# Optimization experiments

Measured on AMD Instinct MI355X. Metric: run time of the kernel, lower is better.

Reference implementation:

```python
import jax, jax.numpy as jnp
import numpy as np

T, B, E, H, V = 50, 64, 1024, 1024, 32000
NL = 2


def setup_inputs() -> dict:
    key = jax.random.key(0)
    ks = jax.random.split(key, 16)
    def rn(k, shape, fan_in):
        return jax.random.normal(k, shape, jnp.float32) * (1.0 / np.sqrt(fan_in))
    return {
        "word": jax.random.randint(ks[0], (B,), 0, V),
        "seq": jax.random.randint(ks[1], (T, B), 0, V),
        "emb": jax.random.normal(ks[2], (V, E), jnp.float32) * 0.05,
        "w2h_W": rn(ks[3], (H, E), E),
        "w2h_b": jnp.zeros((H,), jnp.float32),
        "W_ih0": rn(ks[4], (4 * H, 2 * E), 2 * E),
        "W_hh0": rn(ks[5], (4 * H, H), H),
        "b_ih0": jnp.zeros((4 * H,), jnp.float32),
        "b_hh0": jnp.zeros((4 * H,), jnp.float32),
        "W_ih1": rn(ks[6], (4 * H, H), H),
        "W_hh1": rn(ks[7], (4 * H, H), H),
        "b_ih1": jnp.zeros((4 * H,), jnp.float32),
        "b_hh1": jnp.zeros((4 * H,), jnp.float32),
        "dec_W": rn(ks[8], (V, H), H),
        "dec_b": jnp.zeros((V,), jnp.float32),
    }


def _lstm_layer(x, Wih, Whh, bih, bhh, h0, c0):
    """x: [T,B,D] -> hs: [T,B,H]. PyTorch gate order: i,f,g,o."""
    b = bih + bhh
    # precompute input contribution for all timesteps (one big GEMM)
    xg = jnp.einsum('tbd,gd->tbg', x, Wih) + b  # [T,B,4H]

    def step(carry, xt):
        h, c = carry
        gates = xt + h @ Whh.T
        i, f, g, o = jnp.split(gates, 4, axis=-1)
        c = jax.nn.sigmoid(f) * c + jax.nn.sigmoid(i) * jnp.tanh(g)
        h = jax.nn.sigmoid(o) * jnp.tanh(c)
        return (h, c), h

    (hT, cT), hs = jax.lax.scan(step, (h0, c0), xg)
    return hs, hT, cT


def reference(word, seq, emb, w2h_W, w2h_b, W_ih0, W_hh0, b_ih0, b_hh0,
              W_ih1, W_hh1, b_ih1, b_hh1, dec_W, dec_b):
    word_emb = emb[word]            # [B,E]
    seq_emb = emb[seq]              # [T,B,E]
    # init_hidden: c = word2hidden(word_emb) expanded over layers, h = zeros
    c0 = word_emb @ w2h_W.T + w2h_b          # [B,H]
    h0 = jnp.zeros_like(c0)
    # use_input: concat word_emb to every timestep input
    x0 = jnp.concatenate(
        [jnp.broadcast_to(word_emb[None], (T, B, E)), seq_emb], axis=-1)  # [T,B,2E]
    hs0, h0T, c0T = _lstm_layer(x0, W_ih0, W_hh0, b_ih0, b_hh0, h0, c0)
    hs1, h1T, c1T = _lstm_layer(hs0, W_ih1, W_hh1, b_ih1, b_hh1, h0, c0)
    outputs = hs1.reshape(T * B, H)
    decoded = outputs @ dec_W.T + dec_b      # [T*B, V]
    h_final = jnp.stack([h0T, h1T], 0)       # [NL,B,H]
    c_final = jnp.stack([c0T, c1T], 0)
    return decoded, h_final, c_final
```

## Files before the change

### kernel.cpp

```cpp
#include <hip/hip_runtime.h>
#include <cstddef>


static constexpr int T_ = 50, B_ = 64, E_ = 1024, H_ = 1024, V_ = 32000;
static constexpr int G_ = 4096;

typedef unsigned short u16;
typedef unsigned int u32;
typedef unsigned long long u64;
typedef __attribute__((ext_vector_type(8))) short bf16x8;
typedef __attribute__((ext_vector_type(8))) unsigned short u16x8;
typedef __attribute__((ext_vector_type(4))) float f32x4;

__device__ __forceinline__ int perm_g(int n) {
  return ((n >> 4) & 3) * H_ + (n >> 6) * 16 + (n & 15);
}
__device__ __forceinline__ u16 bf16_rn(float x) {
  union { float f; unsigned u; } a; a.f = x;
  unsigned r = a.u + 0x7fffu + ((a.u >> 16) & 1u);
  return (u16)(r >> 16);
}
__device__ __forceinline__ float bf16_f(u16 h) {
  union { float f; unsigned u; } a; a.u = ((unsigned)h) << 16;
  return a.f;
}
__device__ __forceinline__ float sigm(float x) { return 1.f / (1.f + __expf(-x)); }

__global__ void fill_zero(float* p, int n) {
  int i = blockIdx.x * blockDim.x + threadIdx.x;
  if (i < n) p[i] = 0.f;
}
__global__ void bias_perm(const float* a, const float* b, float* dst) {
  int n = blockIdx.x * 256 + threadIdx.x;
  int s = perm_g(n);
  dst[n] = a[s] + b[s];
}

__global__ void conv_w(const float* __restrict__ src, int srcld, int coloff,
                       const int* __restrict__ gidx, int PERM, int rows,
                       u16* __restrict__ dst) {
  int idx = blockIdx.x * 256 + threadIdx.x;
  int r = idx >> 7, kc = (idx & 127) << 3;
  if (r >= rows) return;
  int s = gidx ? gidx[r] : (PERM ? perm_g(r) : r);
  const float* p = src + (size_t)s * srcld + coloff + kc;
  float4 v0 = *(const float4*)p, v1 = *(const float4*)(p + 4);
  float vv[8] = {v0.x, v0.y, v0.z, v0.w, v1.x, v1.y, v1.z, v1.w};
  u16 hi[8], lo[8];
#pragma unroll
  for (int i = 0; i < 8; ++i) {
    hi[i] = bf16_rn(vv[i]);
    lo[i] = bf16_rn(vv[i] - bf16_f(hi[i]));
  }
  u16x8 c0, c1;
#pragma unroll
  for (int i = 0; i < 4; ++i) {
    c0[2 * i] = hi[i];     c0[2 * i + 1] = lo[i];
    c1[2 * i] = hi[4 + i]; c1[2 * i + 1] = lo[4 + i];
  }
  int seg = kc >> 5;
  int ch0 = (kc >> 2) & 7;
  size_t base = (size_t)r * 2048 + seg * 64;
  *(u16x8*)&dst[base + (size_t)((ch0 ^ (r & 7)) << 3)] = c0;
  *(u16x8*)&dst[base + (size_t)(((ch0 | 1) ^ (r & 7)) << 3)] = c1;
}

template<int BM, int BN, int BK, int TM, int TN>
__launch_bounds__(256)
__global__ void gemm_nt(
    const float* __restrict__ A, const int* __restrict__ Aidx, int lda,
    const float* __restrict__ W, int ldw, int koff,
    const float* __restrict__ bias, float* __restrict__ C, int ldc,
    int M, int N, int K) {
  constexpr int TX = BN / TN;
  constexpr int TY = BM / TM;
  static_assert(TX * TY == 256, "thread geometry");
  __shared__ float As[BK][BM + 4];
  __shared__ float Ws[BK][BN + 4];
  const int tid = threadIdx.x;
  const int tx = tid % TX, ty = tid / TX;
  const int m0 = blockIdx.y * BM, n0 = blockIdx.x * BN;
  float acc[TM][TN];
#pragma unroll
  for (int i = 0; i < TM; ++i)
#pragma unroll
    for (int j = 0; j < TN; ++j) acc[i][j] = 0.f;
  constexpr int AV = (BM * BK) / 4;
  constexpr int WV = (BN * BK) / 4;
  constexpr int KV = BK / 4;
  for (int k0 = 0; k0 < K; k0 += BK) {
#pragma unroll
    for (int lp = 0; lp < (AV + 255) / 256; ++lp) {
      int e = tid + lp * 256;
      if (e < AV) {
        int r = e / KV, kq = e % KV;
        int m = m0 + r;
        float4 v = make_float4(0.f, 0.f, 0.f, 0.f);
        if (m < M) {
          int row = Aidx ? Aidx[m] : m;
          v = *(const float4*)&A[(size_t)row * lda + k0 + kq * 4];
        }
        As[kq * 4 + 0][r] = v.x; As[kq * 4 + 1][r] = v.y;
        As[kq * 4 + 2][r] = v.z; As[kq * 4 + 3][r] = v.w;
      }
    }
#pragma unroll
    for (int lp = 0; lp < (WV + 255) / 256; ++lp) {
      int e = tid + lp * 256;
      if (e < WV) {
        int cc = e / KV, kq = e % KV;
        int n = n0 + cc;
        float4 v = make_float4(0.f, 0.f, 0.f, 0.f);
        if (n < N)
          v = *(const float4*)&W[(size_t)n * ldw + koff + k0 + kq * 4];
        Ws[kq * 4 + 0][cc] = v.x; Ws[kq * 4 + 1][cc] = v.y;
        Ws[kq * 4 + 2][cc] = v.z; Ws[kq * 4 + 3][cc] = v.w;
      }
    }
    __syncthreads();
#pragma unroll
    for (int kk = 0; kk < BK; ++kk) {
      float a[TM], b[TN];
#pragma unroll
      for (int i = 0; i < TM; ++i) a[i] = As[kk][ty * TM + i];
#pragma unroll
      for (int j = 0; j < TN; ++j) b[j] = Ws[kk][tx * TN + j];
#pragma unroll
      for (int i = 0; i < TM; ++i)
#pragma unroll
        for (int j = 0; j < TN; ++j)
          acc[i][j] += a[i] * b[j];
    }
    __syncthreads();
  }
#pragma unroll
  for (int i = 0; i < TM; ++i) {
    int m = m0 + ty * TM + i;
    if (m >= M) continue;
#pragma unroll
    for (int j = 0; j < TN; ++j) {
      int n = n0 + tx * TN + j;
      if (n >= N) continue;
      float v = acc[i][j];
      if (bias) v += bias[n];
      C[(size_t)m * ldc + n] = v;
    }
  }
}

__launch_bounds__(256)
__global__ void gemm_bt(const u16* __restrict__ A, int Mrows,
                        const u16* __restrict__ Wb,
                        const float* __restrict__ bias,
                        const float* __restrict__ Dadd, int ldd, int dmask,
                        float* __restrict__ C, int ldc, int N, int nbx,
                        int mt, int ord) {
  __shared__ u16 lsA[128 * 64];
  __shared__ u16 lsB[128 * 64];

  int nwg = gridDim.x, bid = blockIdx.x;
  int q = nwg >> 3, r = nwg & 7;
  int xcd = bid & 7, base = bid >> 3;
  int wg = (xcd < r ? xcd * (q + 1) : r * (q + 1) + (xcd - r) * q) + base;
  int bx, by;
  if (ord) { by = wg % mt; bx = wg / mt; } else { bx = wg % nbx; by = wg / nbx; }
  const int m0 = by * 128, n0 = bx * 128;

  const int tid = threadIdx.x, w = tid >> 6, l = tid & 63;
  const int lr = l & 15, lq = l >> 4;
  const int wm = (w >> 1) * 64, wn = (w & 1) * 64;

  f32x4 acc[4][4] = {};

  for (int kt = 0; kt < 32; ++kt) {
#pragma unroll
    for (int i = 0; i < 4; ++i) {
      int rb = w * 32 + i * 8;
      int gm = m0 + rb + (l >> 3);
      if (gm > Mrows - 1) gm = Mrows - 1;
      const u16* ga = A + (size_t)gm * 2048 + kt * 64 + (l & 7) * 8;
      __builtin_amdgcn_global_load_lds(
          (const __attribute__((address_space(1))) void*)ga,
          (__attribute__((address_space(3))) void*)(lsA + rb * 64), 16, 0, 0);
      const u16* gb = Wb + (size_t)(n0 + rb + (l >> 3)) * 2048 + kt * 64 + (l & 7) * 8;
      __builtin_amdgcn_global_load_lds(
          (const __attribute__((address_space(1))) void*)gb,
          (__attribute__((address_space(3))) void*)(lsB + rb * 64), 16, 0, 0);
    }
    asm volatile("s_waitcnt vmcnt(0)" ::: "memory");
    __syncthreads();

    bf16x8 af[4][2], bfr[4][2];
#pragma unroll
    for (int i = 0; i < 4; ++i) {
      int ar = wm + i * 16 + lr;
#pragma unroll
      for (int s = 0; s < 2; ++s)
        af[i][s] = *(const bf16x8*)&lsA[ar * 64 + (((s << 2) + lq) ^ (ar & 7)) * 8];
    }
#pragma unroll
    for (int j = 0; j < 4; ++j) {
      int br = wn + j * 16 + lr;
#pragma unroll
      for (int s = 0; s < 2; ++s)
        bfr[j][s] = *(const bf16x8*)&lsB[br * 64 + (((s << 2) + lq) ^ (br & 7)) * 8];
    }
#pragma unroll
    for (int i = 0; i < 4; ++i)
#pragma unroll
      for (int j = 0; j < 4; ++j) {
        acc[i][j] = __builtin_amdgcn_mfma_f32_16x16x32_bf16(af[i][0], bfr[j][0], acc[i][j], 0, 0, 0);
        acc[i][j] = __builtin_amdgcn_mfma_f32_16x16x32_bf16(af[i][1], bfr[j][1], acc[i][j], 0, 0, 0);
      }
    __syncthreads();
  }

#pragma unroll
  for (int i = 0; i < 4; ++i) {
    int mbase = m0 + wm + i * 16 + lq * 4;
#pragma unroll
    for (int j = 0; j < 4; ++j) {
      int n = n0 + wn + j * 16 + lr;
      float badd = bias ? bias[n] : 0.f;
#pragma unroll
      for (int rr = 0; rr < 4; ++rr) {
        int m = mbase + rr;
        if (m >= Mrows) continue;
        float v = acc[i][j][rr] + badd;
        if (Dadd) {
          int dr = (dmask < 0) ? m : (m & dmask);
          v += Dadd[(size_t)dr * ldd + n];
        }
        C[(size_t)m * ldc + n] = v;
      }
    }
  }
}

__launch_bounds__(256)
__global__ void gemm_sp(
    const float* __restrict__ A, int lda,
    const float* __restrict__ W, int ldw,
    const float* __restrict__ bias,
    float* __restrict__ C, int ldc, int M, int N, int K, int nbx) {
  __shared__ u16 As_h[128][40], As_l[128][40];
  __shared__ u16 Ws_h[128][40], Ws_l[128][40];
  int nwg = gridDim.x, bid = blockIdx.x;
  int q = nwg >> 3, r = nwg & 7;
  int xcd = bid & 7, base = bid >> 3;
  int wg = (xcd < r ? xcd * (q + 1) : r * (q + 1) + (xcd - r) * q) + base;
  int bx = wg % nbx, by = wg / nbx;
  const int m0 = by * 128, n0 = bx * 128;
  const int tid = threadIdx.x;
  const int wave = tid >> 6, lane = tid & 63;
  const int lr = lane & 15, lq = lane >> 4;
  const int wm = (wave >> 1) * 64, wn = (wave & 1) * 64;
  f32x4 acc[4][4] = {};
  for (int k0 = 0; k0 < K; k0 += 32) {
#pragma unroll
    for (int lp = 0; lp < 4; ++lp) {
      int s = tid + lp * 256;
      int row = s >> 3, kq = s & 7;
      float4 v = make_float4(0.f, 0.f, 0.f, 0.f);
      int gm = m0 + row;
      if (gm < M)
        v = *(const float4*)&A[(size_t)gm * lda + k0 + kq * 4];
      u16 h0 = bf16_rn(v.x), h1 = bf16_rn(v.y), h2 = bf16_rn(v.z), h3 = bf16_rn(v.w);
      u16 l0 = bf16_rn(v.x - bf16_f(h0)), l1 = bf16_rn(v.y - bf16_f(h1));
      u16 l2 = bf16_rn(v.z - bf16_f(h2)), l3 = bf16_rn(v.w - bf16_f(h3));
      *(uint2*)&As_h[row][kq * 4] =
          make_uint2((u32)h0 | ((u32)h1 << 16), (u32)h2 | ((u32)h3 << 16));
      *(uint2*)&As_l[row][kq * 4] =
          make_uint2((u32)l0 | ((u32)l1 << 16), (u32)l2 | ((u32)l3 << 16));
    }
#pragma unroll
    for (int lp = 0; lp < 4; ++lp) {
      int s = tid + lp * 256;
      int col = s >> 3, kq = s & 7;
      int n = n0 + col;
      float4 v = make_float4(0.f, 0.f, 0.f, 0.f);
      if (n < N)
        v = *(const float4*)&W[(size_t)n * ldw + k0 + kq * 4];
      u16 h0 = bf16_rn(v.x), h1 = bf16_rn(v.y), h2 = bf16_rn(v.z), h3 = bf16_rn(v.w);
      u16 l0 = bf16_rn(v.x - bf16_f(h0)), l1 = bf16_rn(v.y - bf16_f(h1));
      u16 l2 = bf16_rn(v.z - bf16_f(h2)), l3 = bf16_rn(v.w - bf16_f(h3));
      *(uint2*)&Ws_h[col][kq * 4] =
          make_uint2((u32)h0 | ((u32)h1 << 16), (u32)h2 | ((u32)h3 << 16));
      *(uint2*)&Ws_l[col][kq * 4] =
          make_uint2((u32)l0 | ((u32)l1 << 16), (u32)l2 | ((u32)l3 << 16));
    }
    __syncthreads();
    bf16x8 ah[4], al[4], bh[4], bl[4];
#pragma unroll
    for (int i = 0; i < 4; ++i) {
      ah[i] = *(const bf16x8*)&As_h[wm + i * 16 + lr][lq * 8];
      al[i] = *(const bf16x8*)&As_l[wm + i * 16 + lr][lq * 8];
    }
#pragma unroll
    for (int j = 0; j < 4; ++j) {
      bh[j] = *(const bf16x8*)&Ws_h[wn + j * 16 + lr][lq * 8];
      bl[j] = *(const bf16x8*)&Ws_l[wn + j * 16 + lr][lq * 8];
    }
#pragma unroll
    for (int i = 0; i < 4; ++i)
#pragma unroll
      for (int j = 0; j < 4; ++j) {
        acc[i][j] = __builtin_amdgcn_mfma_f32_16x16x32_bf16(ah[i], bh[j], acc[i][j], 0, 0, 0);
        acc[i][j] = __builtin_amdgcn_mfma_f32_16x16x32_bf16(ah[i], bl[j], acc[i][j], 0, 0, 0);
        acc[i][j] = __builtin_amdgcn_mfma_f32_16x16x32_bf16(al[i], bh[j], acc[i][j], 0, 0, 0);
      }
    __syncthreads();
  }
#pragma unroll
  for (int i = 0; i < 4; ++i) {
    int mbase = m0 + wm + i * 16 + lq * 4;
#pragma unroll
    for (int j = 0; j < 4; ++j) {
      int n = n0 + wn + j * 16 + lr;
      if (n >= N) continue;
      float badd = bias ? bias[n] : 0.f;
#pragma unroll
      for (int rr = 0; rr < 4; ++rr) {
        int m = mbase + rr;
        if (m >= M) continue;
        C[(size_t)m * ldc + n] = acc[i][j][rr] + badd;
      }
    }
  }
}

__device__ __forceinline__ void gemm_half(
    const u32* __restrict__ hp, int rg, int w, int lr, int lq,
    const bf16x8 (&bfr)[8][4], f32x4 (&acc)[2][4]) {
  bf16x8 af[8][2];
#pragma unroll
  for (int s = 0; s < 8; ++s)
#pragma unroll
    for (int mt = 0; mt < 2; ++mt) {
      int m = rg * 32 + mt * 16 + lr;
      int seg = w * 4 + (s >> 1);
      int cis = ((((s & 1) << 2) + lq) ^ (lr & 7));
      const u32* p = hp + (size_t)m * 1024 + seg * 32 + cis * 4;
      asm volatile("global_load_dwordx4 %0, %1, off sc0 sc1"
                   : "=v"(af[s][mt]) : "v"(p) : "memory");
    }
  asm volatile("s_waitcnt vmcnt(0)" ::: "memory");
  __builtin_amdgcn_sched_barrier(0);
#pragma unroll
  for (int s = 0; s < 8; ++s)
#pragma unroll
    for (int mt = 0; mt < 2; ++mt)
#pragma unroll
      for (int nt = 0; nt < 4; ++nt)
        acc[mt][nt] = __builtin_amdgcn_mfma_f32_16x16x32_bf16(
            af[s][mt], bfr[s][nt], acc[mt][nt], 0, 0, 0);
}

__device__ __forceinline__ void poll_flags(const u32* flags, int rg, int l, u32 tgt) {
  int guard = 0;
  for (;;) {
    u32 v = __hip_atomic_load(flags + (size_t)((rg << 6) + l) * 4,
                              __ATOMIC_RELAXED, __HIP_MEMORY_SCOPE_AGENT);
    if (__all(v >= tgt)) break;
    if (++guard > (1 << 23)) break;
    __builtin_amdgcn_s_sleep(1);
  }
}

__device__ void decoder_block(char* smem, int dblk,
                              const u32* __restrict__ h1s,
                              const float* __restrict__ decW,
                              const float* __restrict__ dec_b,
                              const u32* __restrict__ flg1,
                              float* __restrict__ outC, int tid) {
  u16* As = (u16*)smem;
  u16* Bs = (u16*)(smem + 32768);
  const int w = tid >> 6, l = tid & 63;
  const int lr = l & 15, lq = l >> 4;
  const int n0 = dblk * 128;
  const u16* h1u = (const u16*)h1s;
  const int wmL = (w >> 1) * 64, wnL = (w & 1) * 64;

  for (int ch = 0; ch < 13; ++ch) {
    const int nSl = (ch < 12) ? 4 : 2;
    const int nrows = nSl * 64;
    const u32 tgt = (u32)(4 * ch + nSl);
    if (w == 0) { poll_flags(flg1, 0, l, tgt); poll_flags(flg1, 1, l, tgt); }
    __syncthreads();

    f32x4 acc[4][4] = {};
    for (int kt = 0; kt < 32; ++kt) {
#pragma unroll
      for (int i = 0; i < 4; ++i) {
        int rb = w * 32 + i * 8;
        int rl = rb + (l >> 3);
        int gm = rl < nrows ? rl : nrows - 1;
        int slot = 4 * ch + 1 + (gm >> 6);
        const u16* ga = h1u + (size_t)slot * (64 * 2048) +
                        (size_t)(gm & 63) * 2048 + kt * 64 + (l & 7) * 8;
        __builtin_amdgcn_global_load_lds(
            (const __attribute__((address_space(1))) void*)ga,
            (__attribute__((address_space(3))) void*)(As + rb * 64), 16, 0, 0);
      }
      {
        int row = tid >> 2, kq8 = (tid & 3) * 8;
        const float* p = decW + (size_t)(n0 + row) * 1024 + kt * 32 + kq8;
        float4 v0 = *(const float4*)p, v1 = *(const float4*)(p + 4);
        float vv[8] = {v0.x, v0.y, v0.z, v0.w, v1.x, v1.y, v1.z, v1.w};
        u16 hi[8], lo[8];
#pragma unroll
        for (int q2 = 0; q2 < 8; ++q2) {
          hi[q2] = bf16_rn(vv[q2]);
          lo[q2] = bf16_rn(vv[q2] - bf16_f(hi[q2]));
        }
        u16x8 c0, c1;
#pragma unroll
        for (int q2 = 0; q2 < 4; ++q2) {
          c0[2 * q2] = hi[q2];     c0[2 * q2 + 1] = lo[q2];
          c1[2 * q2] = hi[4 + q2]; c1[2 * q2 + 1] = lo[4 + q2];
        }
        int c0i = kq8 >> 2;
        u16* dst = Bs + row * 64;
        *(u16x8*)&dst[(c0i ^ (row & 7)) << 3] = c0;
        *(u16x8*)&dst[((c0i | 1) ^ (row & 7)) << 3] = c1;
      }
      asm volatile("s_waitcnt vmcnt(0)" ::: "memory");
      __syncthreads();

      bf16x8 af[4][2], bfr[4][2];
#pragma unroll
      for (int i = 0; i < 4; ++i) {
        int ar = wmL + i * 16 + lr;
#pragma unroll
        for (int s = 0; s < 2; ++s)
          af[i][s] = *(const bf16x8*)&As[ar * 64 + (((s << 2) + lq) ^ (ar & 7)) * 8];
      }
#pragma unroll
      for (int j = 0; j < 4; ++j) {
        int br = wnL + j * 16 + lr;
#pragma unroll
        for (int s = 0; s < 2; ++s)
          bfr[j][s] = *(const bf16x8*)&Bs[br * 64 + (((s << 2) + lq) ^ (br & 7)) * 8];
      }
#pragma unroll
      for (int i = 0; i < 4; ++i)
#pragma unroll
        for (int j = 0; j < 4; ++j) {
          acc[i][j] = __builtin_amdgcn_mfma_f32_16x16x32_bf16(af[i][0], bfr[j][0], acc[i][j], 0, 0, 0);
          acc[i][j] = __builtin_amdgcn_mfma_f32_16x16x32_bf16(af[i][1], bfr[j][1], acc[i][j], 0, 0, 0);
        }
      __syncthreads();
    }
#pragma unroll
    for (int i = 0; i < 4; ++i) {
      int mrow = wmL + i * 16 + lq * 4;
      if (mrow >= nrows) continue;
#pragma unroll
      for (int j = 0; j < 4; ++j) {
        int col = n0 + wnL + j * 16 + lr;
        float badd = dec_b[col];
#pragma unroll
        for (int rr = 0; rr < 4; ++rr)
          outC[(size_t)(ch * 256 + mrow + rr) * V_ + col] = acc[i][j][rr] + badd;
      }
    }
  }
}

template<bool DUAL, bool EMIT, bool DEC>
__launch_bounds__(512, 4)
__global__ void rnn_dual(const u16* __restrict__ Whh0b, const u16* __restrict__ Whh1b,
                         const u16* __restrict__ Wih1b,
                         const float* __restrict__ xg0all, const float* __restrict__ bias1p,
                         float* __restrict__ cL0, float* __restrict__ hL0,
                         float* __restrict__ cL1, float* __restrict__ hL1,
                         u32* __restrict__ h0s, u32* __restrict__ h1s,
                         float* __restrict__ hsf,
                         u32* __restrict__ flg0, u32* __restrict__ flg1,
                         const float* __restrict__ decW, const float* __restrict__ dec_b,
                         float* __restrict__ outC, int T) {
  __shared__ char smem[69632];
  float* partial = (float*)smem;

  const int bid = blockIdx.x;
  const int tid = threadIdx.x, w = tid >> 6, l = tid & 63;
  const int lr = l & 15, lq = l >> 4;

  if (DEC && bid >= 256) {
    decoder_block(smem, bid - 256, h1s, decW, dec_b, flg1, outC, tid);
    return;
  }

  const int x = bid & 7, j = bid >> 3;
  const int layer = DUAL ? (j & 1) : 0;
  const int idx = DUAL ? (j >> 1) : j;
  const int ct = x * 8 + (idx & 7);
  const int rg = idx >> 3;

  const u16* WbA = (layer ? Whh1b : Whh0b) + (size_t)(ct * 64) * 2048;
  bf16x8 bfragA[8][4];
#pragma unroll
  for (int s = 0; s < 8; ++s)
#pragma unroll
    for (int nt = 0; nt < 4; ++nt) {
      int row = nt * 16 + lr;
      int seg = w * 4 + (s >> 1);
      int cis = ((((s & 1) << 2) + lq) ^ (lr & 7));
      bfragA[s][nt] = *(const bf16x8*)&WbA[(size_t)row * 2048 + seg * 64 + cis * 8];
    }
  bf16x8 bfragX[8][4];
  if (DUAL && layer) {
    const u16* WbX = Wih1b + (size_t)(ct * 64) * 2048;
#pragma unroll
    for (int s = 0; s < 8; ++s)
#pragma unroll
      for (int nt = 0; nt < 4; ++nt) {
        int row = nt * 16 + lr;
        int seg = w * 4 + (s >> 1);
        int cis = ((((s & 1) << 2) + lq) ^ (lr & 7));
        bfragX[s][nt] = *(const bf16x8*)&WbX[(size_t)row * 2048 + seg * 64 + cis * 8];
      }
  }

  const int cm = tid >> 4, cu = tid & 15;
  const int m_c = rg * 32 + cm;
  const int unit = ct * 16 + cu;
  float* cL = layer ? cL1 : cL0;
  float* hL = layer ? hL1 : hL0;
  u32* hsl = layer ? h1s : h0s;
  u32* flgS = layer ? flg1 : flg0;
  float creg = cL[m_c * H_ + unit];
  float bset[4];
  if (layer) {
#pragma unroll
    for (int g = 0; g < 4; ++g)
      bset[g] = bias1p[ct * 64 + g * 16 + cu];
  }

  for (int t = 0; t < T; ++t) {
    float xgv[4];
    if (!layer) {
      const float* xg = xg0all + (size_t)t * ((size_t)B_ * G_);
#pragma unroll
      for (int g = 0; g < 4; ++g)
        xgv[g] = xg[(size_t)m_c * G_ + ct * 64 + g * 16 + cu];
    } else {
#pragma unroll
      for (int g = 0; g < 4; ++g) xgv[g] = bset[g];
    }

    f32x4 acc[2][4] = {};

    if (layer) {
      if (t && w == 0) poll_flags(flg1, rg, l, (u32)t);
      __syncthreads();
      gemm_half(h1s + (size_t)t * (B_ * 1024), rg, w, lr, lq, bfragA, acc);
      if (w == 0) poll_flags(flg0, rg, l, (u32)(t + 1));
      __syncthreads();
      gemm_half(h0s + (size_t)(t + 1) * (B_ * 1024), rg, w, lr, lq, bfragX, acc);
    } else {
      if (t && w == 0) poll_flags(flg0, rg, l, (u32)t);
      __syncthreads();
      gemm_half(h0s + (size_t)t * (B_ * 1024), rg, w, lr, lq, bfragA, acc);
    }

#pragma unroll
    for (int mt = 0; mt < 2; ++mt)
#pragma unroll
      for (int nt = 0; nt < 4; ++nt)
#pragma unroll
        for (int rr = 0; rr < 4; ++rr)
          partial[(w * 32 + mt * 16 + lq * 4 + rr) * 68 + nt * 16 + lr] = acc[mt][nt][rr];
    __syncthreads();

    float g4[4];
#pragma unroll
    for (int g = 0; g < 4; ++g) {
      float ssum = xgv[g];
#pragma unroll
      for (int p = 0; p < 8; ++p) ssum += partial[(p * 32 + cm) * 68 + g * 16 + cu];
      g4[g] = ssum;
    }
    float cn = sigm(g4[1]) * creg + sigm(g4[0]) * tanhf(g4[2]);
    float hn = sigm(g4[3]) * tanhf(cn);
    creg = cn;
    if (EMIT && layer) hsf[(size_t)t * (B_ * H_) + m_c * H_ + unit] = hn;
    if (t == T - 1) { cL[m_c * H_ + unit] = cn; hL[m_c * H_ + unit] = hn; }
    u16 hh = bf16_rn(hn);
    u16 hl2 = bf16_rn(hn - bf16_f(hh));
    u32 packed = (u32)hh | ((u32)hl2 << 16);
    u32* hnext = hsl + (size_t)(t + 1) * (B_ * 1024);
    u32 hidx = m_c * 1024 + ((unit >> 5) << 5) +
               ((((unit >> 2) & 7) ^ (m_c & 7)) << 2) + (unit & 3);
    {
      u32* sp = hnext + hidx;
      asm volatile("global_store_dword %0, %1, off sc0 sc1"
                   :: "v"(sp), "v"(packed) : "memory");
    }

    asm volatile("s_waitcnt vmcnt(0)" ::: "memory");
    __syncthreads();
    if (tid == 0)
      __hip_atomic_store(flgS + (size_t)((rg << 6) + ct) * 4, (u32)(t + 1),
                         __ATOMIC_RELAXED, __HIP_MEMORY_SCOPE_AGENT);
  }
}

__launch_bounds__(256)
__global__ void rnn_step(const u16* __restrict__ hprev, const u16* __restrict__ Wb,
                         const float* __restrict__ xg,
                         float* __restrict__ c, float* __restrict__ hf,
                         u32* __restrict__ hout) {
  __shared__ char smem[32768];
  u16* lsA = (u16*)smem;
  u16* lsB = (u16*)(smem + 16384);
  const int nt = blockIdx.x, n0 = nt * 64;
  const int tid = threadIdx.x, w = tid >> 6, l = tid & 63;
  const int lr = l & 15, lq = l >> 4;
  f32x4 acc[4] = {};
  for (int kt = 0; kt < 16; ++kt) {
#pragma unroll
    for (int i = 0; i < 4; ++i) {
      int rb = w * 16 + i * 4;
      const u16* ga = hprev + (size_t)(rb + (l >> 4)) * 2048 + kt * 128 + (l & 15) * 8;
      __builtin_amdgcn_global_load_lds(
          (const __attribute__((address_space(1))) void*)ga,
          (__attribute__((address_space(3))) void*)(lsA + rb * 128), 16, 0, 0);
      const u16* gb = Wb + (size_t)(n0 + rb + (l >> 4)) * 2048 + kt * 128 + (l & 15) * 8;
      __builtin_amdgcn_global_load_lds(
          (const __attribute__((address_space(1))) void*)gb,
          (__attribute__((address_space(3))) void*)(lsB + rb * 128), 16, 0, 0);
    }
    asm volatile("s_waitcnt vmcnt(0)" ::: "memory");
    __syncthreads();
    bf16x8 af[4];
    int ar = w * 16 + lr;
#pragma unroll
    for (int s = 0; s < 4; ++s)
      af[s] = *(const bf16x8*)&lsA[ar * 128 + (s >> 1) * 64 + ((((s & 1) << 2) + lq) ^ (ar & 7)) * 8];
#pragma unroll
    for (int jj = 0; jj < 4; ++jj) {
      int br = jj * 16 + lr;
#pragma unroll
      for (int s = 0; s < 4; ++s) {
        bf16x8 bv = *(const bf16x8*)&lsB[br * 128 + (s >> 1) * 64 + ((((s & 1) << 2) + lq) ^ (br & 7)) * 8];
        acc[jj] = __builtin_amdgcn_mfma_f32_16x16x32_bf16(af[s], bv, acc[jj], 0, 0, 0);
      }
    }
    __syncthreads();
  }
  float* gsh = (float*)smem;
#pragma unroll
  for (int jj = 0; jj < 4; ++jj)
#pragma unroll
    for (int rr = 0; rr < 4; ++rr)
      gsh[(w * 16 + lq * 4 + rr) * 68 + jj * 16 + lr] = acc[jj][rr];
  __syncthreads();
  const int ui = tid & 15, mq = tid >> 4;
#pragma unroll
  for (int mr = 0; mr < 4; ++mr) {
    int m = mr * 16 + mq;
    float gi = gsh[m * 68 + 0 + ui]  + xg[(size_t)m * G_ + n0 + 0 + ui];
    float gf = gsh[m * 68 + 16 + ui] + xg[(size_t)m * G_ + n0 + 16 + ui];
    float gg = gsh[m * 68 + 32 + ui] + xg[(size_t)m * G_ + n0 + 32 + ui];
    float go = gsh[m * 68 + 48 + ui] + xg[(size_t)m * G_ + n0 + 48 + ui];
    int unit = nt * 16 + ui;
    int ci = m * H_ + unit;
    float cn = sigm(gf) * c[ci] + sigm(gi) * tanhf(gg);
    float hn = sigm(go) * tanhf(cn);
    c[ci] = cn;
    hf[ci] = hn;
    u16 hh = bf16_rn(hn);
    u16 hl = bf16_rn(hn - bf16_f(hh));
    u32 hidx = m * 1024 + ((unit >> 5) << 5) +
               ((((unit >> 2) & 7) ^ (m & 7)) << 2) + (unit & 3);
    hout[hidx] = (u32)hh | ((u32)hl << 16);
  }
}

extern "C" void kernel_launch(void* const* d_in, const int* in_sizes, int n_in,
                              void* d_out, int out_size, void* d_ws, size_t ws_size,
                              hipStream_t stream) {
  const int*   word  = (const int*)  d_in[0];
  const int*   seq   = (const int*)  d_in[1];
  const float* emb   = (const float*)d_in[2];
  const float* w2h_W = (const float*)d_in[3];
  const float* w2h_b = (const float*)d_in[4];
  const float* W_ih0 = (const float*)d_in[5];
  const float* W_hh0 = (const float*)d_in[6];
  const float* b_ih0 = (const float*)d_in[7];
  const float* b_hh0 = (const float*)d_in[8];
  const float* W_ih1 = (const float*)d_in[9];
  const float* W_hh1 = (const float*)d_in[10];
  const float* b_ih1 = (const float*)d_in[11];
  const float* b_hh1 = (const float*)d_in[12];
  const float* dec_W = (const float*)d_in[13];
  const float* dec_b = (const float*)d_in[14];

  float* out = (float*)d_out;
  float* hL0 = out + 102400000;
  float* hL1 = hL0 + B_ * H_;
  float* cL0 = out + 102531072;
  float* cL1 = cL0 + B_ * H_;

  u16*   x0w_bf   = (u16*)(out + 13200000);
  u16*   x0seq_bf = (u16*)(out + 13300000);
  u16*   wih0a_bf = (u16*)(out + 20000000);
  u16*   wih0b_bf = (u16*)(out + 24200000);
  float* y_w      = out + 73800000;
  float* bias0p   = out + 74400000;

  const size_t need0    = 129600000;
  const size_t need_hs1 = (size_t)T_ * B_ * H_ * 4;
  const bool tier0 = ws_size >= need0;
  const bool tier2 = !tier0 && ws_size >= need_hs1;

  if (tier0) {
    char* wsb = (char*)d_ws;
    u32*   h1p    = (u32*)wsb;
    u32*   h0p    = (u32*)(wsb + 13369344);
    float* xg0p   = (float*)(wsb + 26738688);
    u16*   whh0p  = (u16*)(wsb + 79167488);
    u16*   whh1p  = (u16*)(wsb + 95944704);
    u16*   wih1p  = (u16*)(wsb + 112721920);
    float* b1p    = (float*)(wsb + 129499136);
    u32*   f0p    = (u32*)(wsb + 129515520);
    u32*   f1p    = (u32*)(wsb + 129519616);

    fill_zero<<<8, 256, 0, stream>>>((float*)f0p, 2048);
    fill_zero<<<256, 256, 0, stream>>>((float*)h0p, 65536);
    fill_zero<<<256, 256, 0, stream>>>((float*)h1p, 65536);
    bias_perm<<<16, 256, 0, stream>>>(b_ih0, b_hh0, bias0p);
    bias_perm<<<16, 256, 0, stream>>>(b_ih1, b_hh1, b1p);

    gemm_nt<64, 64, 16, 4, 4><<<dim3(16, 1), 256, 0, stream>>>(
        emb, word, E_, w2h_W, E_, 0, w2h_b, cL0, H_, B_, H_, E_);
    gemm_nt<64, 64, 16, 4, 4><<<dim3(16, 1), 256, 0, stream>>>(
        emb, word, E_, w2h_W, E_, 0, w2h_b, cL1, H_, B_, H_, E_);

    conv_w<<<2048, 256, 0, stream>>>(W_ih0, 2 * E_, 0,  nullptr, 1, G_, wih0a_bf);
    conv_w<<<2048, 256, 0, stream>>>(W_ih0, 2 * E_, E_, nullptr, 1, G_, wih0b_bf);
    conv_w<<<2048, 256, 0, stream>>>(W_ih1, H_, 0, nullptr, 1, G_, wih1p);
    conv_w<<<2048, 256, 0, stream>>>(W_hh0, H_, 0, nullptr, 1, G_, whh0p);
    conv_w<<<2048, 256, 0, stream>>>(W_hh1, H_, 0, nullptr, 1, G_, whh1p);
    conv_w<<<32,   256, 0, stream>>>(emb, E_, 0, word, 0, B_, x0w_bf);
    conv_w<<<1600, 256, 0, stream>>>(emb, E_, 0, seq, 0, T_ * B_, x0seq_bf);

    gemm_bt<<<32, 256, 0, stream>>>(x0w_bf, B_, wih0a_bf, bias0p,
                                    nullptr, 0, -1, y_w, G_, G_, 32, 1, 0);
    gemm_bt<<<800, 256, 0, stream>>>(x0seq_bf, T_ * B_, wih0b_bf, nullptr,
                                     y_w, G_, 63, xg0p, G_, G_, 32, 25, 0);

    rnn_dual<true, false, true><<<506, 512, 0, stream>>>(
        whh0p, whh1p, wih1p, xg0p, b1p,
        cL0, hL0, cL1, hL1, h0p, h1p, nullptr, f0p, f1p,
        dec_W, dec_b, out, T_);
  } else {
    float* xg0      = out;
    u32*   hs0slots = (u32*)(out + 16600000);
    u16*   wih1_bf  = (u16*)(out + 28400000);
    u16*   whh0_bf  = (u16*)(out + 32600000);
    u16*   whh1_bf  = (u16*)(out + 36800000);
    float* bias1p   = out + 74410000;
    float* xg1      = out + 87560192;
    u32*   h1alt    = (u32*)(out + 91000000);
    u32*   flg0     = (u32*)(out + 101000000);
    u32*   flg1     = (u32*)(out + 101004096);
    u32*   hbfA     = (u32*)(out + 101100000);
    u32*   hbfB     = (u32*)(out + 101200000);
    float* hs1f     = (float*)d_ws;

    fill_zero<<<32, 256, 0, stream>>>(out + 101000000, 8192);
    fill_zero<<<256, 256, 0, stream>>>((float*)hs0slots, 65536);
    if (tier2) fill_zero<<<256, 256, 0, stream>>>((float*)h1alt, 65536);
    bias_perm<<<16, 256, 0, stream>>>(b_ih0, b_hh0, bias0p);
    bias_perm<<<16, 256, 0, stream>>>(b_ih1, b_hh1, bias1p);

    gemm_nt<64, 64, 16, 4, 4><<<dim3(16, 1), 256, 0, stream>>>(
        emb, word, E_, w2h_W, E_, 0, w2h_b, cL0, H_, B_, H_, E_);
    gemm_nt<64, 64, 16, 4, 4><<<dim3(16, 1), 256, 0, stream>>>(
        emb, word, E_, w2h_W, E_, 0, w2h_b, cL1, H_, B_, H_, E_);

    conv_w<<<2048, 256, 0, stream>>>(W_ih0, 2 * E_, 0,  nullptr, 1, G_, wih0a_bf);
    conv_w<<<2048, 256, 0, stream>>>(W_ih0, 2 * E_, E_, nullptr, 1, G_, wih0b_bf);
    conv_w<<<2048, 256, 0, stream>>>(W_ih1, H_, 0, nullptr, 1, G_, wih1_bf);
    conv_w<<<2048, 256, 0, stream>>>(W_hh0, H_, 0, nullptr, 1, G_, whh0_bf);
    conv_w<<<2048, 256, 0, stream>>>(W_hh1, H_, 0, nullptr, 1, G_, whh1_bf);
    conv_w<<<32,   256, 0, stream>>>(emb, E_, 0, word, 0, B_, x0w_bf);
    conv_w<<<1600, 256, 0, stream>>>(emb, E_, 0, seq, 0, T_ * B_, x0seq_bf);

    gemm_bt<<<32, 256, 0, stream>>>(x0w_bf, B_, wih0a_bf, bias0p,
                                    nullptr, 0, -1, y_w, G_, G_, 32, 1, 0);
    gemm_bt<<<800, 256, 0, stream>>>(x0seq_bf, T_ * B_, wih0b_bf, nullptr,
                                     y_w, G_, 63, xg0, G_, G_, 32, 25, 0);

    if (tier2) {
      rnn_dual<true, true, false><<<256, 512, 0, stream>>>(
          whh0_bf, whh1_bf, wih1_bf, xg0, bias1p,
          cL0, hL0, cL1, hL1, hs0slots, h1alt, hs1f, flg0, flg1,
          nullptr, nullptr, nullptr, T_);
      gemm_sp<<<6250, 256, 0, stream>>>(
          hs1f, H_, dec_W, H_, dec_b, out, V_, T_ * B_, V_, H_, 250);
    } else {
      rnn_dual<false, false, false><<<128, 512, 0, stream>>>(
          whh0_bf, whh1_bf, wih1_bf, xg0, bias1p,
          cL0, hL0, cL1, hL1, hs0slots, nullptr, nullptr, flg0, flg1,
          nullptr, nullptr, nullptr, T_);
      gemm_bt<<<800, 256, 0, stream>>>((const u16*)(hs0slots + (size_t)B_ * 1024),
                                       T_ * B_, wih1_bf, bias1p,
                                       nullptr, 0, -1, xg1, G_, G_, 32, 25, 0);
      for (int t = 0; t < T_; ++t) {
        const u16* hp = t ? (const u16*)((t & 1) ? hbfA : hbfB) : (const u16*)hs0slots;
        u32* ho = (t & 1) ? hbfB : hbfA;
        rnn_step<<<64, 256, 0, stream>>>(
            hp, whh1_bf, xg1 + (size_t)t * B_ * G_, cL1, hL1, ho);
        gemm_sp<<<250, 256, 0, stream>>>(
            hL1, H_, dec_W, H_, dec_b, out + (size_t)t * B_ * V_, V_, B_, V_, H_, 250);
      }
    }
  }
}
```

Measured before the change: 2.156 ms.

## Per-wave flag polling, finer decoder chunks, and merged c0 GEMM

In the recurrent kernel, each wave now polls only the eight producer flags it depends on, replacing the wave-0 poll followed by a block-wide barrier. This is meant to cut synchronisation latency on the per-timestep critical path. The fused decoder now consumes 128-row chunks (two timesteps) instead of 256, so it can start sooner and overlap more with the recurrence, with a retiled MFMA layout. The two identical word2hidden GEMMs are merged into one launch that writes both outputs, and the launch_bounds occupancy hint drops from 4 to 1, which may change register allocation.

```diff
diff --git a/kernel.cpp b/kernel.cpp
--- a/kernel.cpp
+++ b/kernel.cpp
@@ -70,8 +70,8 @@
 __global__ void gemm_nt(
     const float* __restrict__ A, const int* __restrict__ Aidx, int lda,
     const float* __restrict__ W, int ldw, int koff,
-    const float* __restrict__ bias, float* __restrict__ C, int ldc,
-    int M, int N, int K) {
+    const float* __restrict__ bias, float* __restrict__ C, float* __restrict__ C2,
+    int ldc, int M, int N, int K) {
   constexpr int TX = BN / TN;
   constexpr int TY = BM / TM;
   static_assert(TX * TY == 256, "thread geometry");
@@ -144,6 +144,7 @@
       float v = acc[i][j];
       if (bias) v += bias[n];
       C[(size_t)m * ldc + n] = v;
+      if (C2) C2[(size_t)m * ldc + n] = v;
     }
   }
 }
@@ -356,6 +357,19 @@
             af[s][mt], bfr[s][nt], acc[mt][nt], 0, 0, 0);
 }
 
+__device__ __forceinline__ void poll_src(const u32* flags, int rg, int w, int l, u32 tgt) {
+  int guard = 0;
+  for (;;) {
+    u32 v = tgt;
+    if (l < 8)
+      v = __hip_atomic_load(flags + (size_t)((rg << 6) + (w << 3) + l) * 4,
+                            __ATOMIC_RELAXED, __HIP_MEMORY_SCOPE_AGENT);
+    if (__all(v >= tgt)) break;
+    if (++guard > (1 << 23)) break;
+    __builtin_amdgcn_s_sleep(1);
+  }
+}
+
 __device__ __forceinline__ void poll_flags(const u32* flags, int rg, int l, u32 tgt) {
   int guard = 0;
   for (;;) {
@@ -379,25 +393,22 @@
   const int lr = l & 15, lq = l >> 4;
   const int n0 = dblk * 128;
   const u16* h1u = (const u16*)h1s;
-  const int wmL = (w >> 1) * 64, wnL = (w & 1) * 64;
-
-  for (int ch = 0; ch < 13; ++ch) {
-    const int nSl = (ch < 12) ? 4 : 2;
-    const int nrows = nSl * 64;
-    const u32 tgt = (u32)(4 * ch + nSl);
+  const int wr = w >> 1, wc = w & 1;
+
+  for (int ch = 0; ch < 25; ++ch) {
+    const u32 tgt = (u32)(2 * ch + 2);
     if (w == 0) { poll_flags(flg1, 0, l, tgt); poll_flags(flg1, 1, l, tgt); }
     __syncthreads();
 
-    f32x4 acc[4][4] = {};
+    f32x4 acc[2][4] = {};
     for (int kt = 0; kt < 32; ++kt) {
 #pragma unroll
-      for (int i = 0; i < 4; ++i) {
-        int rb = w * 32 + i * 8;
-        int rl = rb + (l >> 3);
-        int gm = rl < nrows ? rl : nrows - 1;
-        int slot = 4 * ch + 1 + (gm >> 6);
+      for (int i = 0; i < 2; ++i) {
+        int rb = w * 16 + i * 8;
+        int grow = rb + (l >> 3);
+        int slot = 2 * ch + 1 + (grow >> 6);
         const u16* ga = h1u + (size_t)slot * (64 * 2048) +
-                        (size_t)(gm & 63) * 2048 + kt * 64 + (l & 7) * 8;
+                        (size_t)(grow & 63) * 2048 + kt * 64 + (l & 7) * 8;
         __builtin_amdgcn_global_load_lds(
             (const __attribute__((address_space(1))) void*)ga,
             (__attribute__((address_space(3))) void*)(As + rb * 64), 16, 0, 0);
@@ -427,48 +438,48 @@
       asm volatile("s_waitcnt vmcnt(0)" ::: "memory");
       __syncthreads();
 
-      bf16x8 af[4][2], bfr[4][2];
-#pragma unroll
-      for (int i = 0; i < 4; ++i) {
-        int ar = wmL + i * 16 + lr;
+      bf16x8 af[2][2], bfr[2][4];
+#pragma unroll
+      for (int mt = 0; mt < 2; ++mt) {
+        int ar = wr * 32 + mt * 16 + lr;
 #pragma unroll
         for (int s = 0; s < 2; ++s)
-          af[i][s] = *(const bf16x8*)&As[ar * 64 + (((s << 2) + lq) ^ (ar & 7)) * 8];
-      }
-#pragma unroll
-      for (int j = 0; j < 4; ++j) {
-        int br = wnL + j * 16 + lr;
+          af[mt][s] = *(const bf16x8*)&As[ar * 64 + (((s << 2) + lq) ^ (ar & 7)) * 8];
+      }
+#pragma unroll
+      for (int nt = 0; nt < 4; ++nt) {
+        int br = wc * 64 + nt * 16 + lr;
 #pragma unroll
         for (int s = 0; s < 2; ++s)
-          bfr[j][s] = *(const bf16x8*)&Bs[br * 64 + (((s << 2) + lq) ^ (br & 7)) * 8];
-      }
-#pragma unroll
-      for (int i = 0; i < 4; ++i)
-#pragma unroll
-        for (int j = 0; j < 4; ++j) {
-          acc[i][j] = __builtin_amdgcn_mfma_f32_16x16x32_bf16(af[i][0], bfr[j][0], acc[i][j], 0, 0, 0);
-          acc[i][j] = __builtin_amdgcn_mfma_f32_16x16x32_bf16(af[i][1], bfr[j][1], acc[i][j], 0, 0, 0);
-        }
+          bfr[s][nt] = *(const bf16x8*)&Bs[br * 64 + (((s << 2) + lq) ^ (br & 7)) * 8];
+      }
+#pragma unroll
+      for (int s = 0; s < 2; ++s)
+#pragma unroll
+        for (int mt = 0; mt < 2; ++mt)
+#pragma unroll
+          for (int nt = 0; nt < 4; ++nt)
+            acc[mt][nt] = __builtin_amdgcn_mfma_f32_16x16x32_bf16(
+                af[mt][s], bfr[s][nt], acc[mt][nt], 0, 0, 0);
       __syncthreads();
     }
 #pragma unroll
-    for (int i = 0; i < 4; ++i) {
-      int mrow = wmL + i * 16 + lq * 4;
-      if (mrow >= nrows) continue;
-#pragma unroll
-      for (int j = 0; j < 4; ++j) {
-        int col = n0 + wnL + j * 16 + lr;
+    for (int mt = 0; mt < 2; ++mt) {
+      int mrow0 = wr * 32 + mt * 16 + lq * 4;
+#pragma unroll
+      for (int nt = 0; nt < 4; ++nt) {
+        int col = n0 + wc * 64 + nt * 16 + lr;
         float badd = dec_b[col];
 #pragma unroll
         for (int rr = 0; rr < 4; ++rr)
-          outC[(size_t)(ch * 256 + mrow + rr) * V_ + col] = acc[i][j][rr] + badd;
+          outC[(size_t)(ch * 128 + mrow0 + rr) * V_ + col] = acc[mt][nt][rr] + badd;
       }
     }
   }
 }
 
 template<bool DUAL, bool EMIT, bool DEC>
-__launch_bounds__(512, 4)
+__launch_bounds__(512, 1)
 __global__ void rnn_dual(const u16* __restrict__ Whh0b, const u16* __restrict__ Whh1b,
                          const u16* __restrict__ Wih1b,
                          const float* __restrict__ xg0all, const float* __restrict__ bias1p,
@@ -552,15 +563,12 @@
     f32x4 acc[2][4] = {};
 
     if (layer) {
-      if (t && w == 0) poll_flags(flg1, rg, l, (u32)t);
-      __syncthreads();
+      if (t) poll_src(flg1, rg, w, l, (u32)t);
       gemm_half(h1s + (size_t)t * (B_ * 1024), rg, w, lr, lq, bfragA, acc);
-      if (w == 0) poll_flags(flg0, rg, l, (u32)(t + 1));
-      __syncthreads();
+      poll_src(flg0, rg, w, l, (u32)(t + 1));
       gemm_half(h0s + (size_t)(t + 1) * (B_ * 1024), rg, w, lr, lq, bfragX, acc);
     } else {
-      if (t && w == 0) poll_flags(flg0, rg, l, (u32)t);
-      __syncthreads();
+      if (t) poll_src(flg0, rg, w, l, (u32)t);
       gemm_half(h0s + (size_t)t * (B_ * 1024), rg, w, lr, lq, bfragA, acc);
     }
 
@@ -734,9 +742,7 @@
     bias_perm<<<16, 256, 0, stream>>>(b_ih1, b_hh1, b1p);
 
     gemm_nt<64, 64, 16, 4, 4><<<dim3(16, 1), 256, 0, stream>>>(
-        emb, word, E_, w2h_W, E_, 0, w2h_b, cL0, H_, B_, H_, E_);
-    gemm_nt<64, 64, 16, 4, 4><<<dim3(16, 1), 256, 0, stream>>>(
-        emb, word, E_, w2h_W, E_, 0, w2h_b, cL1, H_, B_, H_, E_);
+        emb, word, E_, w2h_W, E_, 0, w2h_b, cL0, cL1, H_, B_, H_, E_);
 
     conv_w<<<2048, 256, 0, stream>>>(W_ih0, 2 * E_, 0,  nullptr, 1, G_, wih0a_bf);
     conv_w<<<2048, 256, 0, stream>>>(W_ih0, 2 * E_, E_, nullptr, 1, G_, wih0b_bf);
@@ -777,9 +783,7 @@
     bias_perm<<<16, 256, 0, stream>>>(b_ih1, b_hh1, bias1p);
 
     gemm_nt<64, 64, 16, 4, 4><<<dim3(16, 1), 256, 0, stream>>>(
-        emb, word, E_, w2h_W, E_, 0, w2h_b, cL0, H_, B_, H_, E_);
-    gemm_nt<64, 64, 16, 4, 4><<<dim3(16, 1), 256, 0, stream>>>(
-        emb, word, E_, w2h_W, E_, 0, w2h_b, cL1, H_, B_, H_, E_);
+        emb, word, E_, w2h_W, E_, 0, w2h_b, cL0, cL1, H_, B_, H_, E_);
 
     conv_w<<<2048, 256, 0, stream>>>(W_ih0, 2 * E_, 0,  nullptr, 1, G_, wih0a_bf);
     conv_w<<<2048, 256, 0, stream>>>(W_ih0, 2 * E_, E_, nullptr, 1, G_, wih0b_bf);
```

Result: slower. 2.262 ms (+5.0%).
